# Performance work log

Hardware: AMD Instinct MI355X
Metric: run time of the kernel (lower is better)

Reference implementation:

```python
import jax, jax.numpy as jnp
import numpy as np

S = 3072      # total packed tokens
D = 1536      # hidden_size
H = 12        # num_heads
HD = D // H   # head_dim = 128
NSEQ = 4      # number of packed sequences (images)


def rotate_half(x):
    x1 = x[..., : x.shape[-1] // 2]
    x2 = x[..., x.shape[-1] // 2 :]
    return jnp.concatenate((-x2, x1), axis=-1)


def setup_inputs() -> dict:
    key = jax.random.key(0)
    k1, k2, k3 = jax.random.split(key, 3)
    hidden_states = jax.random.normal(k1, (S, D), jnp.float32)
    # 4 equal-length packed sequences
    cu_seqlens = (jnp.arange(NSEQ + 1, dtype=jnp.int32) * (S // NSEQ))
    # RoPE cos/sin per token, period within each packed sequence
    pos = (jnp.arange(S) % (S // NSEQ)).astype(jnp.float32)
    inv_freq = 1.0 / (10000.0 ** (jnp.arange(0, HD // 2, dtype=jnp.float32) / (HD // 2)))
    freqs = pos[:, None] * inv_freq[None, :]          # [S, HD//2]
    emb = jnp.concatenate([freqs, freqs], axis=-1)    # [S, HD]
    cos, sin = jnp.cos(emb), jnp.sin(emb)
    qkv_w = jax.random.normal(k2, (3 * D, D), jnp.float32) * (D ** -0.5)
    qkv_b = jnp.zeros((3 * D,), jnp.float32)
    proj_w = jax.random.normal(k3, (D, D), jnp.float32) * (D ** -0.5)
    return {
        "hidden_states": hidden_states,
        "cos": cos,
        "sin": sin,
        "qkv_w": qkv_w,
        "qkv_b": qkv_b,
        "proj_w": proj_w,
        "cu_seqlens": cu_seqlens,
    }


def reference(hidden_states, cos, sin, qkv_w, qkv_b, proj_w, cu_seqlens):
    s_len, dim = hidden_states.shape
    # fused QKV projection -> [S, 3, H, HD]
    qkv = (hidden_states @ qkv_w.T + qkv_b).reshape(s_len, 3, H, HD)
    q, k, v = qkv[:, 0], qkv[:, 1], qkv[:, 2]         # each [S, H, HD]
    # inline RoPE (fp32, broadcast over heads)
    c = cos[:, None, :].astype(jnp.float32)
    s = sin[:, None, :].astype(jnp.float32)
    qf, kf = q.astype(jnp.float32), k.astype(jnp.float32)
    q = (qf * c + rotate_half(qf) * s).astype(q.dtype)
    k = (kf * c + rotate_half(kf) * s).astype(k.dtype)
    # block-diagonal (varlen) mask from cu_seqlens
    seg = jnp.searchsorted(cu_seqlens, jnp.arange(s_len), side="right")  # [S]
    same_seq = seg[:, None] == seg[None, :]                              # [S, S]
    bias = jnp.where(same_seq, 0.0, -jnp.inf).astype(jnp.float32)
    scaling = HD ** -0.5
    # scores [H, S, S]
    scores = jnp.einsum("shd,thd->hst", q, k) * scaling + bias[None]
    probs = jax.nn.softmax(scores.astype(jnp.float32), axis=-1).astype(q.dtype)
    attn = jnp.einsum("hst,thd->shd", probs, v).reshape(s_len, dim)
    return attn @ proj_w.T
```

## Files before the change

### kernel.cpp

```cpp
#include <hip/hip_runtime.h>
#include <stdint.h>

#define S_LEN 3072
#define DIM   1536
#define NH    12
#define HD    128
#define QKV_N 4608

typedef unsigned short u16;
typedef __bf16 bf16x8 __attribute__((ext_vector_type(8)));
typedef float  f32x4  __attribute__((ext_vector_type(4)));
typedef u16    u16x8  __attribute__((ext_vector_type(8)));

#define AS1 __attribute__((address_space(1)))
#define AS3 __attribute__((address_space(3)))
#define GLL16(g, l) __builtin_amdgcn_global_load_lds((AS1 void*)(g), (AS3 void*)(l), 16, 0, 0)

__device__ __forceinline__ u16 f2bf(float f) {
  unsigned u = __float_as_uint(f);
  u = (u + 0x7fffu + ((u >> 16) & 1u)) >> 16;
  return (u16)u;
}
__device__ __forceinline__ float bf2f(u16 b) {
  return __uint_as_float(((unsigned)b) << 16);
}

__global__ __launch_bounds__(256) void cvt_bf16_3(const float* __restrict__ in0, u16* __restrict__ out0, int n0,
                                                  const float* __restrict__ in1, u16* __restrict__ out1, int n1,
                                                  const float* __restrict__ in2, u16* __restrict__ out2, int n2) {
  int total = n0 + n1 + n2;
  int stride = gridDim.x * blockDim.x;
  for (int i = blockIdx.x * blockDim.x + threadIdx.x; i < total; i += stride) {
    const float* src; u16* dst; int j;
    if (i < n0)           { src = in0; dst = out0; j = i; }
    else if (i < n0 + n1) { src = in1; dst = out1; j = i - n0; }
    else                  { src = in2; dst = out2; j = i - n0 - n1; }
    float4 v = ((const float4*)src)[j];
    ushort4 o;
    o.x = f2bf(v.x); o.y = f2bf(v.y); o.z = f2bf(v.z); o.w = f2bf(v.w);
    ((ushort4*)dst)[j] = o;
  }
}


__device__ __forceinline__ bf16x8 frag2(const u16* region, int row, int ch) {
  int L = row >> 1;
  int slot = ((ch + ((row & 1) << 2)) ^ L) & 7;
  return *(const bf16x8*)(region + L * 64 + slot * 8);
}

__global__ __launch_bounds__(512, 2) void gemm_bt_256(const u16* __restrict__ A,
                                                      const u16* __restrict__ B,
                                                      const float* __restrict__ bias,
                                                      u16* __restrict__ Cout,
                                                      int M, int N, int K) {
  __shared__ __attribute__((aligned(16))) u16 lds[8 * 8192];

  const int t = threadIdx.x;
  const int l = t & 63;
  const int w = t >> 6;
  const int wm = w >> 2;
  const int wn = w & 3;
  const int lr = l & 15;
  const int lc = l >> 4;

  const int nbx = N >> 8;
  const int nwg = gridDim.x;
  const int q = nwg >> 3, r = nwg & 7;
  const int xcd = blockIdx.x & 7, rest = blockIdx.x >> 3;
  const int wgid = (xcd < r ? xcd * (q + 1) : r * (q + 1) + (xcd - r) * q) + rest;
  const int m0 = (wgid / nbx) * 256;
  const int n0 = (wgid % nbx) * 256;

  const int nk = K >> 6;

  f32x4 acc[8][4];
  #pragma unroll
  for (int i = 0; i < 8; ++i)
    #pragma unroll
    for (int j = 0; j < 4; ++j) acc[i][j] = f32x4{0.f, 0.f, 0.f, 0.f};

  auto stage_half = [&](int buf, int ks, int ab, int kt) {
    const u16* base = ab ? B : A;
    const int x0 = ab ? n0 : m0;
    u16* dst = lds + (((buf << 2) | (ks << 1) | ab) * 8192);
    #pragma unroll
    for (int i = 0; i < 2; ++i) {
      int C = t + i * 512;
      int L = C >> 3, s = C & 7;
      int u = s ^ (L & 7);
      int row = 2 * L + (u >> 2), ch = u & 3;
      const u16* src = base + (size_t)(x0 + row) * K + kt * 64 + ks * 32 + ch * 8;
      GLL16(src, dst + C * 8);
    }
  };

  stage_half(0, 0, 0, 0); stage_half(0, 0, 1, 0);
  stage_half(0, 1, 0, 0); stage_half(0, 1, 1, 0);
  if (nk > 1) { stage_half(1, 0, 0, 1); stage_half(1, 0, 1, 1); }
  asm volatile("s_waitcnt vmcnt(4)" ::: "memory");
  __builtin_amdgcn_s_barrier();

  for (int kt = 0; kt < nk; ++kt) {
    const int buf = kt & 1, nbuf = buf ^ 1;
    const bool st1 = (kt + 1 < nk);
    const bool st2 = (kt + 2 < nk);

    const u16* A0 = lds + (((buf << 2) | 0) * 8192);
    const u16* B0 = lds + (((buf << 2) | 1) * 8192);
    const u16* A1 = lds + (((buf << 2) | 2) * 8192);
    const u16* B1 = lds + (((buf << 2) | 3) * 8192);

    bf16x8 bfrag[4], afr[4];

    #pragma unroll
    for (int ni = 0; ni < 4; ++ni) bfrag[ni] = frag2(B0, wn * 64 + ni * 16 + lr, lc);
    #pragma unroll
    for (int mi = 0; mi < 4; ++mi) afr[mi] = frag2(A0, wm * 128 + mi * 16 + lr, lc);
    if (st1) stage_half(nbuf, 1, 0, kt + 1);
    __builtin_amdgcn_s_barrier();
    __builtin_amdgcn_s_setprio(1);
    #pragma unroll
    for (int mi = 0; mi < 4; ++mi)
      #pragma unroll
      for (int ni = 0; ni < 4; ++ni)
        acc[mi][ni] = __builtin_amdgcn_mfma_f32_16x16x32_bf16(afr[mi], bfrag[ni],
                                                              acc[mi][ni], 0, 0, 0);
    __builtin_amdgcn_s_setprio(0);
    __builtin_amdgcn_s_barrier();

    #pragma unroll
    for (int mi = 0; mi < 4; ++mi) afr[mi] = frag2(A0, wm * 128 + 64 + mi * 16 + lr, lc);
    if (st1) stage_half(nbuf, 1, 1, kt + 1);
    __builtin_amdgcn_s_barrier();
    __builtin_amdgcn_s_setprio(1);
    #pragma unroll
    for (int mi = 0; mi < 4; ++mi)
      #pragma unroll
      for (int ni = 0; ni < 4; ++ni)
        acc[4 + mi][ni] = __builtin_amdgcn_mfma_f32_16x16x32_bf16(afr[mi], bfrag[ni],
                                                                  acc[4 + mi][ni], 0, 0, 0);
    __builtin_amdgcn_s_setprio(0);
    __builtin_amdgcn_s_barrier();

    #pragma unroll
    for (int ni = 0; ni < 4; ++ni) bfrag[ni] = frag2(B1, wn * 64 + ni * 16 + lr, lc);
    #pragma unroll
    for (int mi = 0; mi < 4; ++mi) afr[mi] = frag2(A1, wm * 128 + mi * 16 + lr, lc);
    if (st2) stage_half(buf, 0, 0, kt + 2);
    __builtin_amdgcn_s_barrier();
    __builtin_amdgcn_s_setprio(1);
    #pragma unroll
    for (int mi = 0; mi < 4; ++mi)
      #pragma unroll
      for (int ni = 0; ni < 4; ++ni)
        acc[mi][ni] = __builtin_amdgcn_mfma_f32_16x16x32_bf16(afr[mi], bfrag[ni],
                                                              acc[mi][ni], 0, 0, 0);
    __builtin_amdgcn_s_setprio(0);
    __builtin_amdgcn_s_barrier();

    #pragma unroll
    for (int mi = 0; mi < 4; ++mi) afr[mi] = frag2(A1, wm * 128 + 64 + mi * 16 + lr, lc);
    if (st2) {
      stage_half(buf, 0, 1, kt + 2);
      asm volatile("s_waitcnt vmcnt(4)" ::: "memory");
    } else if (st1) {
      asm volatile("s_waitcnt vmcnt(0)" ::: "memory");
    }
    __builtin_amdgcn_s_barrier();
    __builtin_amdgcn_s_setprio(1);
    #pragma unroll
    for (int mi = 0; mi < 4; ++mi)
      #pragma unroll
      for (int ni = 0; ni < 4; ++ni)
        acc[4 + mi][ni] = __builtin_amdgcn_mfma_f32_16x16x32_bf16(afr[mi], bfrag[ni],
                                                                  acc[4 + mi][ni], 0, 0, 0);
    __builtin_amdgcn_s_setprio(0);
    __builtin_amdgcn_s_barrier();
  }

  #pragma unroll
  for (int ni = 0; ni < 4; ++ni) {
    int col = n0 + wn * 64 + ni * 16 + lr;
    float bv = bias ? bias[col] : 0.f;
    #pragma unroll
    for (int mi = 0; mi < 8; ++mi) {
      int rbase = m0 + wm * 128 + mi * 16 + (lc << 2);
      #pragma unroll
      for (int rr = 0; rr < 4; ++rr)
        Cout[(size_t)(rbase + rr) * N + col] = f2bf(acc[mi][ni][rr] + bv);
    }
  }
}

__device__ __forceinline__ bf16x8 lds_frag(const u16* base, int row, int ch) {
  return *(const bf16x8*)(base + row * 64 + ((ch ^ row) & 7) * 8);
}

template <bool BIAS, bool OUTF32>
__global__ __launch_bounds__(256) void gemm_bt(const u16* __restrict__ A,
                                               const u16* __restrict__ B,
                                               const float* __restrict__ bias,
                                               void* __restrict__ Cout,
                                               int M, int N, int K) {
  __shared__ u16 Asm[128 * 64];
  __shared__ u16 Bsm[128 * 64];
  const int t = threadIdx.x;
  const int l = t & 63;
  const int w = t >> 6;
  const int wm = w >> 1, wn = w & 1;
  const int m0 = blockIdx.y * 128, n0 = blockIdx.x * 128;

  f32x4 acc[4][4];
  #pragma unroll
  for (int i = 0; i < 4; ++i)
    #pragma unroll
    for (int j = 0; j < 4; ++j) acc[i][j] = f32x4{0.f, 0.f, 0.f, 0.f};

  for (int k0 = 0; k0 < K; k0 += 64) {
    __syncthreads();
    #pragma unroll
    for (int r4 = 0; r4 < 4; ++r4) {
      int C = t + r4 * 256;
      int row = C >> 3, ch = C & 7;
      int sch = (ch ^ row) & 7;
      GLL16(A + (size_t)(m0 + row) * K + k0 + sch * 8, Asm + (size_t)C * 8);
      GLL16(B + (size_t)(n0 + row) * K + k0 + sch * 8, Bsm + (size_t)C * 8);
    }
    __syncthreads();
    #pragma unroll
    for (int ks = 0; ks < 2; ++ks) {
      bf16x8 af[4], bfr[4];
      #pragma unroll
      for (int mi = 0; mi < 4; ++mi)
        af[mi] = lds_frag(Asm, wm * 64 + mi * 16 + (l & 15), ks * 4 + (l >> 4));
      #pragma unroll
      for (int ni = 0; ni < 4; ++ni)
        bfr[ni] = lds_frag(Bsm, wn * 64 + ni * 16 + (l & 15), ks * 4 + (l >> 4));
      #pragma unroll
      for (int mi = 0; mi < 4; ++mi)
        #pragma unroll
        for (int ni = 0; ni < 4; ++ni)
          acc[mi][ni] = __builtin_amdgcn_mfma_f32_16x16x32_bf16(af[mi], bfr[ni],
                                                                acc[mi][ni], 0, 0, 0);
    }
  }

  #pragma unroll
  for (int ni = 0; ni < 4; ++ni) {
    int col = n0 + wn * 64 + ni * 16 + (l & 15);
    float bv = 0.f;
    if (BIAS) bv = bias[col];
    #pragma unroll
    for (int mi = 0; mi < 4; ++mi) {
      int rbase = m0 + wm * 64 + mi * 16 + ((l >> 4) << 2);
      #pragma unroll
      for (int rr = 0; rr < 4; ++rr) {
        float v = acc[mi][ni][rr] + bv;
        if (OUTF32)
          ((float*)Cout)[(size_t)(rbase + rr) * N + col] = v;
        else
          ((u16*)Cout)[(size_t)(rbase + rr) * N + col] = f2bf(v);
      }
    }
  }
}

__global__ __launch_bounds__(256) void rope_pack(const u16* __restrict__ QKV,
                                                 const float* __restrict__ cosb,
                                                 const float* __restrict__ sinb,
                                                 u16* __restrict__ Qp,
                                                 u16* __restrict__ Kp,
                                                 u16* __restrict__ Vt) {
  __shared__ u16 vtile[64][128];
  const int t = threadIdx.x;
  const int s0 = blockIdx.x * 64;
  const int h = blockIdx.y;

  const int srow = s0 + (t >> 2);
  const int d0 = (t & 3) * 16;
  const u16* qkvrow = QKV + (size_t)srow * QKV_N + h * HD;
  const float qscale = 0.08838834764831845f * 1.4426950408889634f;
  #pragma unroll
  for (int which = 0; which < 2; ++which) {
    const u16* src = qkvrow + which * DIM;
    u16* dst = (which ? Kp : Qp) + ((size_t)h * S_LEN + srow) * HD;
    const float sc = which ? 1.f : qscale;
    #pragma unroll
    for (int j = 0; j < 16; ++j) {
      int d = d0 + j;
      float xlo = bf2f(src[d]);
      float xhi = bf2f(src[d + 64]);
      float clo = cosb[srow * HD + d], chi = cosb[srow * HD + d + 64];
      float slo = sinb[srow * HD + d], shi = sinb[srow * HD + d + 64];
      dst[d]      = f2bf((xlo * clo - xhi * slo) * sc);
      dst[d + 64] = f2bf((xhi * chi + xlo * shi) * sc);
    }
  }

  #pragma unroll
  for (int r4 = 0; r4 < 4; ++r4) {
    int C = t + r4 * 256;
    int row = C >> 4, ch = C & 15;
    *(uint4*)(&vtile[row][ch * 8]) =
        *(const uint4*)(QKV + (size_t)(s0 + row) * QKV_N + 2 * DIM + h * HD + ch * 8);
  }
  __syncthreads();
  const int d = t >> 1;
  const int sc0 = (t & 1) * 32;
  u16* vdst = Vt + ((size_t)h * HD + d) * S_LEN + s0 + sc0;
  #pragma unroll
  for (int j = 0; j < 32; j += 8) {
    u16x8 v;
    #pragma unroll
    for (int e = 0; e < 8; ++e) v[e] = vtile[sc0 + j + e][d];
    *(u16x8*)(vdst + j) = v;
  }
}

__global__ __launch_bounds__(256) void attn_fwd(const u16* __restrict__ Qp,
                                                const u16* __restrict__ Kp,
                                                const u16* __restrict__ Vt,
                                                const int* __restrict__ cu,
                                                u16* __restrict__ Obf) {
  __shared__ u16 K_lds[64 * 128];
  __shared__ u16 VT_lds[128 * 64];
  __shared__ u16 P_lds[4][16 * 72];

  const int t = threadIdx.x;
  const int l = t & 63;
  const int w = t >> 6;
  const int q0 = blockIdx.x * 64;
  const int h = blockIdx.y;

  int cs = 0, ce = S_LEN;
  #pragma unroll
  for (int b = 0; b < 4; ++b) {
    int lo = cu[b], hi = cu[b + 1];
    if (q0 >= lo && q0 < hi) { cs = lo; ce = hi; }
  }

  const int qrow = q0 + w * 16 + (l & 15);
  bf16x8 qf[4];
  const u16* qptr = Qp + ((size_t)h * S_LEN + qrow) * HD + ((l >> 4) * 8);
  #pragma unroll
  for (int ks = 0; ks < 4; ++ks) qf[ks] = *(const bf16x8*)(qptr + ks * 32);

  f32x4 acc_o[8];
  #pragma unroll
  for (int i = 0; i < 8; ++i) acc_o[i] = f32x4{0.f, 0.f, 0.f, 0.f};
  float m_run[4], l_run[4];
  #pragma unroll
  for (int r = 0; r < 4; ++r) { m_run[r] = -1e30f; l_run[r] = 0.f; }

  for (int kv0 = cs; kv0 < ce; kv0 += 64) {
    __syncthreads();
    {
      const u16* kbase = Kp + ((size_t)h * S_LEN + kv0) * HD;
      #pragma unroll
      for (int r4 = 0; r4 < 4; ++r4) {
        int C = t + r4 * 256;
        int row = C >> 4, ch = C & 15;
        int sch = (ch & 8) | ((ch ^ row) & 7);
        GLL16(kbase + row * HD + sch * 8, K_lds + (size_t)C * 8);
      }
      const u16* vbase = Vt + (size_t)h * HD * S_LEN + kv0;
      #pragma unroll
      for (int r4 = 0; r4 < 4; ++r4) {
        int C = t + r4 * 256;
        int row = C >> 3, ch = C & 7;
        int sch = (ch ^ row) & 7;
        GLL16(vbase + (size_t)row * S_LEN + sch * 8, VT_lds + (size_t)C * 8);
      }
    }
    __syncthreads();

    f32x4 s_acc[4];
    #pragma unroll
    for (int nf = 0; nf < 4; ++nf) {
      s_acc[nf] = f32x4{0.f, 0.f, 0.f, 0.f};
      int kcol = nf * 16 + (l & 15);
      #pragma unroll
      for (int ks = 0; ks < 4; ++ks) {
        int ch = ks * 4 + (l >> 4);
        int sch = (ch & 8) | ((ch ^ kcol) & 7);
        bf16x8 kf = *(const bf16x8*)(K_lds + kcol * 128 + sch * 8);
        s_acc[nf] = __builtin_amdgcn_mfma_f32_16x16x32_bf16(qf[ks], kf, s_acc[nf], 0, 0, 0);
      }
    }

    float p[4][4], alpha[4];
    #pragma unroll
    for (int r = 0; r < 4; ++r) {
      float v = fmaxf(fmaxf(s_acc[0][r], s_acc[1][r]), fmaxf(s_acc[2][r], s_acc[3][r]));
      #pragma unroll
      for (int m = 1; m < 16; m <<= 1) v = fmaxf(v, __shfl_xor(v, m, 64));
      float mn = fmaxf(m_run[r], v);
      alpha[r] = __builtin_amdgcn_exp2f(m_run[r] - mn);
      m_run[r] = mn;
      float sum = 0.f;
      #pragma unroll
      for (int nf = 0; nf < 4; ++nf) {
        float pv = __builtin_amdgcn_exp2f(s_acc[nf][r] - mn);
        p[nf][r] = pv;
        sum += pv;
      }
      #pragma unroll
      for (int m = 1; m < 16; m <<= 1) sum += __shfl_xor(sum, m, 64);
      l_run[r] = l_run[r] * alpha[r] + sum;
    }
    #pragma unroll
    for (int onf = 0; onf < 8; ++onf)
      #pragma unroll
      for (int r = 0; r < 4; ++r) acc_o[onf][r] *= alpha[r];

    u16* pl = P_lds[w];
    #pragma unroll
    for (int nf = 0; nf < 4; ++nf)
      #pragma unroll
      for (int r = 0; r < 4; ++r)
        pl[((l >> 4) * 4 + r) * 72 + nf * 16 + (l & 15)] = f2bf(p[nf][r]);

    #pragma unroll
    for (int ks = 0; ks < 2; ++ks) {
      bf16x8 pa = *(const bf16x8*)(pl + (l & 15) * 72 + ks * 32 + (l >> 4) * 8);
      #pragma unroll
      for (int onf = 0; onf < 8; ++onf) {
        int d = onf * 16 + (l & 15);
        int ch = ks * 4 + (l >> 4);
        int sch = (ch ^ d) & 7;
        bf16x8 vf = *(const bf16x8*)(VT_lds + d * 64 + sch * 8);
        acc_o[onf] = __builtin_amdgcn_mfma_f32_16x16x32_bf16(pa, vf, acc_o[onf], 0, 0, 0);
      }
    }
  }

  #pragma unroll
  for (int r = 0; r < 4; ++r) {
    float inv = 1.f / l_run[r];
    int srow = q0 + w * 16 + ((l >> 4) << 2) + r;
    u16* orow = Obf + (size_t)srow * DIM + h * HD + (l & 15);
    #pragma unroll
    for (int onf = 0; onf < 8; ++onf) orow[onf * 16] = f2bf(acc_o[onf][r] * inv);
  }
}

extern "C" void kernel_launch(void* const* d_in, const int* in_sizes, int n_in,
                              void* d_out, int out_size, void* d_ws, size_t ws_size,
                              hipStream_t stream) {
  const float* hidden = (const float*)d_in[0];
  const float* cosb   = (const float*)d_in[1];
  const float* sinb   = (const float*)d_in[2];
  const float* qkv_w  = (const float*)d_in[3];
  const float* qkv_b  = (const float*)d_in[4];
  const float* proj_w = (const float*)d_in[5];
  const int*   cu     = (const int*)d_in[6];

  u16* Hbf   = (u16*)d_ws;
  u16* Wqkv  = Hbf   + (size_t)S_LEN * DIM;
  u16* Wproj = Wqkv  + (size_t)QKV_N * DIM;
  u16* QKVbf = Wproj + (size_t)DIM * DIM;
  u16* Kp    = QKVbf + (size_t)S_LEN * QKV_N;
  u16* Vt    = Kp    + (size_t)NH * S_LEN * HD;
  u16* Qp    = Wqkv;
  u16* Abf   = Hbf;

  cvt_bf16_3<<<2048, 256, 0, stream>>>(hidden, Hbf, S_LEN * DIM / 4,
                                       qkv_w, Wqkv, QKV_N * DIM / 4,
                                       proj_w, Wproj, DIM * DIM / 4);

  gemm_bt_256<<<(S_LEN / 256) * (QKV_N / 256), 512, 0, stream>>>(
      Hbf, Wqkv, qkv_b, QKVbf, S_LEN, QKV_N, DIM);

  rope_pack<<<dim3(S_LEN / 64, NH), 256, 0, stream>>>(QKVbf, cosb, sinb, Qp, Kp, Vt);

  attn_fwd<<<dim3(S_LEN / 64, NH), 256, 0, stream>>>(Qp, Kp, Vt, cu, Abf);

  gemm_bt<false, true><<<dim3(DIM / 128, S_LEN / 128), 256, 0, stream>>>(
      Abf, Wproj, nullptr, d_out, S_LEN, DIM, DIM);
}
```

Measured before the change: 169.7 us.

## Double-buffer attention KV loads, stage GEMM epilogue via LDS, vectorize RoPE

After: 174.1 us. 1.03x slower.

```diff
diff --git a/kernel.cpp b/kernel.cpp
--- a/kernel.cpp
+++ b/kernel.cpp
@@ -42,7 +42,6 @@
   }
 }
 
-
 __device__ __forceinline__ bf16x8 frag2(const u16* region, int row, int ch) {
   int L = row >> 1;
   int slot = ((ch + ((row & 1) << 2)) ^ L) & 7;
@@ -179,16 +178,30 @@
     __builtin_amdgcn_s_barrier();
   }
 
-  #pragma unroll
-  for (int ni = 0; ni < 4; ++ni) {
-    int col = n0 + wn * 64 + ni * 16 + lr;
-    float bv = bias ? bias[col] : 0.f;
+  {
+    float bv[4];
+    #pragma unroll
+    for (int ni = 0; ni < 4; ++ni)
+      bv[ni] = bias ? bias[n0 + wn * 64 + ni * 16 + lr] : 0.f;
     #pragma unroll
     for (int mi = 0; mi < 8; ++mi) {
-      int rbase = m0 + wm * 128 + mi * 16 + (lc << 2);
-      #pragma unroll
-      for (int rr = 0; rr < 4; ++rr)
-        Cout[(size_t)(rbase + rr) * N + col] = f2bf(acc[mi][ni][rr] + bv);
+      int row = wm * 128 + mi * 16 + lc * 4;
+      #pragma unroll
+      for (int ni = 0; ni < 4; ++ni) {
+        int scol = (wn * 64 + ni * 16 + lr) ^ (lc << 4);
+        #pragma unroll
+        for (int rr = 0; rr < 4; ++rr)
+          lds[(row + rr) * 256 + scol] = f2bf(acc[mi][ni][rr] + bv[ni]);
+      }
+    }
+    __syncthreads();
+    #pragma unroll
+    for (int i = 0; i < 16; ++i) {
+      int id = i * 512 + t;
+      int row = id >> 5, c16 = id & 31;
+      int s = (row >> 2) & 3;
+      u16x8 v = *(const u16x8*)(lds + row * 256 + ((c16 * 8) ^ (s << 4)));
+      *(u16x8*)(Cout + (size_t)(m0 + row) * N + n0 + c16 * 8) = v;
     }
   }
 }
@@ -281,21 +294,39 @@
   const int d0 = (t & 3) * 16;
   const u16* qkvrow = QKV + (size_t)srow * QKV_N + h * HD;
   const float qscale = 0.08838834764831845f * 1.4426950408889634f;
+
+  float cl[16], chh[16], sl[16], shh[16];
+  #pragma unroll
+  for (int g = 0; g < 4; ++g) {
+    *(float4*)(cl + 4 * g)  = *(const float4*)(cosb + srow * HD + d0 + 4 * g);
+    *(float4*)(chh + 4 * g) = *(const float4*)(cosb + srow * HD + d0 + 64 + 4 * g);
+    *(float4*)(sl + 4 * g)  = *(const float4*)(sinb + srow * HD + d0 + 4 * g);
+    *(float4*)(shh + 4 * g) = *(const float4*)(sinb + srow * HD + d0 + 64 + 4 * g);
+  }
+
   #pragma unroll
   for (int which = 0; which < 2; ++which) {
     const u16* src = qkvrow + which * DIM;
     u16* dst = (which ? Kp : Qp) + ((size_t)h * S_LEN + srow) * HD;
     const float sc = which ? 1.f : qscale;
-    #pragma unroll
-    for (int j = 0; j < 16; ++j) {
-      int d = d0 + j;
-      float xlo = bf2f(src[d]);
-      float xhi = bf2f(src[d + 64]);
-      float clo = cosb[srow * HD + d], chi = cosb[srow * HD + d + 64];
-      float slo = sinb[srow * HD + d], shi = sinb[srow * HD + d + 64];
-      dst[d]      = f2bf((xlo * clo - xhi * slo) * sc);
-      dst[d + 64] = f2bf((xhi * chi + xlo * shi) * sc);
-    }
+    u16x8 xl0 = *(const u16x8*)(src + d0);
+    u16x8 xl1 = *(const u16x8*)(src + d0 + 8);
+    u16x8 xh0 = *(const u16x8*)(src + d0 + 64);
+    u16x8 xh1 = *(const u16x8*)(src + d0 + 72);
+    u16x8 o0, o1, o2, o3;
+    #pragma unroll
+    for (int j = 0; j < 8; ++j) {
+      float xlo = bf2f(xl0[j]), xhi = bf2f(xh0[j]);
+      o0[j] = f2bf((xlo * cl[j] - xhi * sl[j]) * sc);
+      o2[j] = f2bf((xhi * chh[j] + xlo * shh[j]) * sc);
+      float xlo2 = bf2f(xl1[j]), xhi2 = bf2f(xh1[j]);
+      o1[j] = f2bf((xlo2 * cl[j + 8] - xhi2 * sl[j + 8]) * sc);
+      o3[j] = f2bf((xhi2 * chh[j + 8] + xlo2 * shh[j + 8]) * sc);
+    }
+    *(u16x8*)(dst + d0)      = o0;
+    *(u16x8*)(dst + d0 + 8)  = o1;
+    *(u16x8*)(dst + d0 + 64) = o2;
+    *(u16x8*)(dst + d0 + 72) = o3;
   }
 
   #pragma unroll
@@ -323,8 +354,8 @@
                                                 const u16* __restrict__ Vt,
                                                 const int* __restrict__ cu,
                                                 u16* __restrict__ Obf) {
-  __shared__ u16 K_lds[64 * 128];
-  __shared__ u16 VT_lds[128 * 64];
+  __shared__ u16 K_lds[2][64 * 128];
+  __shared__ u16 VT_lds[2][128 * 64];
   __shared__ u16 P_lds[4][16 * 72];
 
   const int t = threadIdx.x;
@@ -353,29 +384,44 @@
   #pragma unroll
   for (int r = 0; r < 4; ++r) { m_run[r] = -1e30f; l_run[r] = 0.f; }
 
-  for (int kv0 = cs; kv0 < ce; kv0 += 64) {
-    __syncthreads();
-    {
-      const u16* kbase = Kp + ((size_t)h * S_LEN + kv0) * HD;
-      #pragma unroll
-      for (int r4 = 0; r4 < 4; ++r4) {
-        int C = t + r4 * 256;
-        int row = C >> 4, ch = C & 15;
-        int sch = (ch & 8) | ((ch ^ row) & 7);
-        GLL16(kbase + row * HD + sch * 8, K_lds + (size_t)C * 8);
-      }
-      const u16* vbase = Vt + (size_t)h * HD * S_LEN + kv0;
-      #pragma unroll
-      for (int r4 = 0; r4 < 4; ++r4) {
-        int C = t + r4 * 256;
-        int row = C >> 3, ch = C & 7;
-        int sch = (ch ^ row) & 7;
-        GLL16(vbase + (size_t)row * S_LEN + sch * 8, VT_lds + (size_t)C * 8);
-      }
-    }
-    __syncthreads();
+  auto stage = [&](int c, int kv0) {
+    const u16* kbase = Kp + ((size_t)h * S_LEN + kv0) * HD;
+    #pragma unroll
+    for (int r4 = 0; r4 < 4; ++r4) {
+      int C = t + r4 * 256;
+      int row = C >> 4, ch = C & 15;
+      int sch = (ch & 8) | ((ch ^ row) & 7);
+      GLL16(kbase + row * HD + sch * 8, &K_lds[c][0] + (size_t)C * 8);
+    }
+    const u16* vbase = Vt + (size_t)h * HD * S_LEN + kv0;
+    #pragma unroll
+    for (int r4 = 0; r4 < 4; ++r4) {
+      int C = t + r4 * 256;
+      int row = C >> 3, ch = C & 7;
+      int sch = (ch ^ row) & 7;
+      GLL16(vbase + (size_t)row * S_LEN + sch * 8, &VT_lds[c][0] + (size_t)C * 8);
+    }
+  };
+
+  const int nt = (ce - cs) >> 6;
+  stage(0, cs);
+
+  for (int it = 0; it < nt; ++it) {
+    const int cur = it & 1;
+    __builtin_amdgcn_s_barrier();
+    if (it + 1 < nt) {
+      stage(cur ^ 1, cs + (it + 1) * 64);
+      asm volatile("s_waitcnt vmcnt(8)" ::: "memory");
+    } else {
+      asm volatile("s_waitcnt vmcnt(0)" ::: "memory");
+    }
+    __builtin_amdgcn_s_barrier();
+
+    const u16* kb = &K_lds[cur][0];
+    const u16* vb = &VT_lds[cur][0];
 
     f32x4 s_acc[4];
+    __builtin_amdgcn_s_setprio(1);
     #pragma unroll
     for (int nf = 0; nf < 4; ++nf) {
       s_acc[nf] = f32x4{0.f, 0.f, 0.f, 0.f};
@@ -384,10 +430,11 @@
       for (int ks = 0; ks < 4; ++ks) {
         int ch = ks * 4 + (l >> 4);
         int sch = (ch & 8) | ((ch ^ kcol) & 7);
-        bf16x8 kf = *(const bf16x8*)(K_lds + kcol * 128 + sch * 8);
+        bf16x8 kf = *(const bf16x8*)(kb + kcol * 128 + sch * 8);
         s_acc[nf] = __builtin_amdgcn_mfma_f32_16x16x32_bf16(qf[ks], kf, s_acc[nf], 0, 0, 0);
       }
     }
+    __builtin_amdgcn_s_setprio(0);
 
     float p[4][4], alpha[4];
     #pragma unroll
@@ -421,6 +468,7 @@
       for (int r = 0; r < 4; ++r)
         pl[((l >> 4) * 4 + r) * 72 + nf * 16 + (l & 15)] = f2bf(p[nf][r]);
 
+    __builtin_amdgcn_s_setprio(1);
     #pragma unroll
     for (int ks = 0; ks < 2; ++ks) {
       bf16x8 pa = *(const bf16x8*)(pl + (l & 15) * 72 + ks * 32 + (l >> 4) * 8);
@@ -429,10 +477,11 @@
         int d = onf * 16 + (l & 15);
         int ch = ks * 4 + (l >> 4);
         int sch = (ch ^ d) & 7;
-        bf16x8 vf = *(const bf16x8*)(VT_lds + d * 64 + sch * 8);
+        bf16x8 vf = *(const bf16x8*)(vb + d * 64 + sch * 8);
         acc_o[onf] = __builtin_amdgcn_mfma_f32_16x16x32_bf16(pa, vf, acc_o[onf], 0, 0, 0);
       }
     }
+    __builtin_amdgcn_s_setprio(0);
   }
 
   #pragma unroll
```
